# Kernel optimization log

Hardware: AMD Instinct MI355X
Metric: run time of the kernel (lower is better)

## Reference

```python
import jax, jax.numpy as jnp
import numpy as np

N_NODES = 40000
N_EDGES = 300000
EMBED = 256
LN_EPS = 1e-5
LEAKY_SLOPE = 0.01


def setup_inputs() -> dict:
    key = jax.random.key(0)
    ks = jax.random.split(key, 5)
    H = jax.random.normal(ks[0], (N_NODES, EMBED), dtype=jnp.float32)
    E = jax.random.normal(ks[1], (N_EDGES, EMBED), dtype=jnp.float32)
    ht = jax.random.randint(ks[2], (N_EDGES, 2), 0, N_NODES, dtype=jnp.int64)
    # Linear weights in torch convention: [out_features, in_features]
    W_fwd = jax.random.normal(ks[3], (EMBED, 2 * EMBED), dtype=jnp.float32) * (1.0 / np.sqrt(2 * EMBED))
    W_back = jax.random.normal(ks[4], (EMBED, 2 * EMBED), dtype=jnp.float32) * (1.0 / np.sqrt(2 * EMBED))
    return {
        "H": H,
        "E": E,
        "ht": ht,
        "queries": jnp.zeros((1,), jnp.float32),            # unused (message_weighting_function=None)
        "influence_weights": jnp.zeros((1,), jnp.float32),  # modeled as None
        "W_fwd": W_fwd,
        "b_fwd": jnp.zeros((EMBED,), jnp.float32),
        "W_back": W_back,
        "b_back": jnp.zeros((EMBED,), jnp.float32),
        "ln_w": jnp.ones((EMBED,), jnp.float32),
        "ln_b": jnp.zeros((EMBED,), jnp.float32),
    }


def _layer_norm(x, w, b):
    mu = jnp.mean(x, axis=-1, keepdims=True)
    var = jnp.mean(jnp.square(x - mu), axis=-1, keepdims=True)  # biased, as torch LayerNorm
    return (x - mu) * jax.lax.rsqrt(var + LN_EPS) * w + b


def reference(H, E, ht, queries, influence_weights, W_fwd, b_fwd, W_back, b_back, ln_w, ln_b):
    # queries / influence_weights are None in the modeled configuration; ignored.
    heads = ht[:, 0]
    tails = ht[:, 1]
    n = H.shape[0]
    # gather -> concat -> linear (messages in both edge directions)
    msg_fwd = jnp.concatenate([H[heads], E], axis=1) @ W_fwd.T + b_fwd    # [m, d]
    msg_back = jnp.concatenate([H[tails], E], axis=1) @ W_back.T + b_back  # [m, d]
    # scatter-add aggregate: fwd messages go to tails, back messages to heads
    msg_dst = jnp.concatenate([tails, heads], axis=0)          # [2m]
    messages = jnp.concatenate([msg_fwd, msg_back], axis=0)    # [2m, d]
    agg = jax.ops.segment_sum(messages, msg_dst, num_segments=n)  # [n, d]
    counts = jax.ops.segment_sum(jnp.ones_like(msg_dst, dtype=H.dtype), msg_dst, num_segments=n)
    agg = agg / counts[:, None]
    out = _layer_norm(jax.nn.leaky_relu(agg, LEAKY_SLOPE) + H, ln_w, ln_b)
    return out
```

## Files before the change

kernel.cpp:

```cpp
#include <hip/hip_runtime.h>
#include <hip/hip_bf16.h>

#define N_NODES 40000
#define N_EDGES 300000
#define EMBED 256
#define CAP 64

typedef __attribute__((ext_vector_type(8))) short s16x8;
typedef __attribute__((ext_vector_type(4))) float f32x4;

__device__ __forceinline__ float b2f(unsigned short u) {
    union { unsigned int i; float f; } v; v.i = ((unsigned int)u) << 16; return v.f;
}
__device__ __forceinline__ unsigned short f2b(float f) {
    unsigned int x = __float_as_uint(f);
    x += 0x7fffu + ((x >> 16) & 1u);
    return (unsigned short)(x >> 16);
}
__device__ __forceinline__ bool ht_is_i64(const int* __restrict__ ht) {
    int o = 0;
    #pragma unroll
    for (int k = 1; k < 16; k += 2) o |= ht[k];
    return o == 0;
}
__device__ __forceinline__ int clampN(int v) {
    unsigned u = (unsigned)v;
    return (u < N_NODES) ? v : 0;
}

__global__ __launch_bounds__(256) void convert_kernel(
    const float* __restrict__ H, const float* __restrict__ Wf,
    const float* __restrict__ Wb,
    unsigned short* __restrict__ Hbf, unsigned short* __restrict__ Wcat)
{
    constexpr int NH4 = (N_NODES * EMBED) / 4;
    constexpr int NW4 = (EMBED * 2 * EMBED) / 4;
    int ci = blockIdx.x * 256 + threadIdx.x;
    const float* src; unsigned short* dst;
    if (ci < NH4) {
        src = &H[(size_t)ci * 4]; dst = &Hbf[(size_t)ci * 4];
    } else if (ci < NH4 + NW4) {
        int j = (ci - NH4) * 4; int n = j >> 9, k = j & 511;
        src = &Wf[j]; dst = &Wcat[(size_t)n * 1024 + k];
    } else if (ci < NH4 + 2 * NW4) {
        int j = (ci - NH4 - NW4) * 4; int n = j >> 9, k = j & 511;
        src = &Wb[j]; dst = &Wcat[(size_t)n * 1024 + 512 + k];
    } else return;
    float4 v = *(const float4*)src;
    ushort4 o; o.x = f2b(v.x); o.y = f2b(v.y); o.z = f2b(v.z); o.w = f2b(v.w);
    *(ushort4*)dst = o;
}

__global__ __launch_bounds__(256) void build_kernel(
    const int* __restrict__ ht,
    int* __restrict__ cntf, int* __restrict__ cntb,
    int* __restrict__ listf, int* __restrict__ listb)
{
    int e = blockIdx.x * 256 + threadIdx.x;
    if (e >= N_EDGES) return;
    const bool wide = ht_is_i64(ht);
    int head = clampN(wide ? ht[(size_t)4 * e]     : ht[2 * e]);
    int tail = clampN(wide ? ht[(size_t)4 * e + 2] : ht[2 * e + 1]);
    int pf = atomicAdd(&cntf[tail], 1);
    if (pf < CAP) listf[tail * CAP + pf] = e;
    int pb = atomicAdd(&cntb[head], 1);
    if (pb < CAP) listb[head * CAP + pb] = e;
}

__global__ __launch_bounds__(256) void fused_kernel(
    const unsigned short* __restrict__ Hbf, const float* __restrict__ E,
    const int* __restrict__ ht, const unsigned short* __restrict__ Wcat,
    const float* __restrict__ bf_, const float* __restrict__ bb_,
    const float* __restrict__ H, const float* __restrict__ lw,
    const float* __restrict__ lb,
    const int* __restrict__ cntf, const int* __restrict__ cntb,
    const int* __restrict__ listf, const int* __restrict__ listb,
    float* __restrict__ out)
{
    constexpr int LDK = 1032;
    __shared__ unsigned short S[16 * LDK];
    __shared__ float stats[16][4][2];

    const int tid  = threadIdx.x;
    const int wid  = tid >> 6;
    const int lane = tid & 63;
    const int q    = lane >> 4;
    const int c    = lane & 15;
    const int m0   = blockIdx.x * 16;
    const bool wide = ht_is_i64(ht);

    for (int i = 0; i < 4; i++) {
        const int r    = wid * 4 + i;
        const int node = m0 + r;
        float aHf[4] = {0.f,0.f,0.f,0.f}, aEf[4] = {0.f,0.f,0.f,0.f};
        float aHb[4] = {0.f,0.f,0.f,0.f}, aEb[4] = {0.f,0.f,0.f,0.f};

        const int nf = min(cntf[node], CAP);
        for (int t = 0; t < nf; t++) {
            int e = listf[node * CAP + t];
            float4 e4 = *(const float4*)(&E[(size_t)e * EMBED + lane * 4]);
            int head = clampN(wide ? ht[(size_t)4 * e] : ht[2 * e]);
            ushort4 h4 = *(const ushort4*)(&Hbf[(size_t)head * EMBED + lane * 4]);
            aHf[0] += b2f(h4.x); aHf[1] += b2f(h4.y); aHf[2] += b2f(h4.z); aHf[3] += b2f(h4.w);
            aEf[0] += e4.x; aEf[1] += e4.y; aEf[2] += e4.z; aEf[3] += e4.w;
        }
        const int nb = min(cntb[node], CAP);
        for (int t = 0; t < nb; t++) {
            int e = listb[node * CAP + t];
            float4 e4 = *(const float4*)(&E[(size_t)e * EMBED + lane * 4]);
            int tail = clampN(wide ? ht[(size_t)4 * e + 2] : ht[2 * e + 1]);
            ushort4 h4 = *(const ushort4*)(&Hbf[(size_t)tail * EMBED + lane * 4]);
            aHb[0] += b2f(h4.x); aHb[1] += b2f(h4.y); aHb[2] += b2f(h4.z); aHb[3] += b2f(h4.w);
            aEb[0] += e4.x; aEb[1] += e4.y; aEb[2] += e4.z; aEb[3] += e4.w;
        }
        ushort4 o;
        o.x=f2b(aHf[0]); o.y=f2b(aHf[1]); o.z=f2b(aHf[2]); o.w=f2b(aHf[3]);
        *(ushort4*)(&S[r * LDK +   0 + lane * 4]) = o;
        o.x=f2b(aEf[0]); o.y=f2b(aEf[1]); o.z=f2b(aEf[2]); o.w=f2b(aEf[3]);
        *(ushort4*)(&S[r * LDK + 256 + lane * 4]) = o;
        o.x=f2b(aHb[0]); o.y=f2b(aHb[1]); o.z=f2b(aHb[2]); o.w=f2b(aHb[3]);
        *(ushort4*)(&S[r * LDK + 512 + lane * 4]) = o;
        o.x=f2b(aEb[0]); o.y=f2b(aEb[1]); o.z=f2b(aEb[2]); o.w=f2b(aEb[3]);
        *(ushort4*)(&S[r * LDK + 768 + lane * 4]) = o;
    }
    __syncthreads();

    const int n0 = wid * 64;
    f32x4 acc[4];
    #pragma unroll
    for (int nt = 0; nt < 4; nt++) acc[nt] = (f32x4){0.f,0.f,0.f,0.f};

    #pragma unroll 4
    for (int k0 = 0; k0 < 1024; k0 += 32) {
        s16x8 a = *(const s16x8*)(&S[c * LDK + k0 + q * 8]);
        #pragma unroll
        for (int nt = 0; nt < 4; nt++) {
            s16x8 b = *(const s16x8*)(&Wcat[(size_t)(n0 + nt * 16 + c) * 1024 + k0 + q * 8]);
            acc[nt] = __builtin_amdgcn_mfma_f32_16x16x32_bf16(a, b, acc[nt], 0, 0, 0);
        }
    }

    float x[4][4];
    float sr[4], ssr[4];
    #pragma unroll
    for (int reg = 0; reg < 4; reg++) {
        const int row  = q * 4 + reg;
        const int node = m0 + row;
        const float cf = (float)cntf[node];
        const float cb = (float)cntb[node];
        const float tot = cf + cb;
        const float inv = (tot > 0.f) ? (1.0f / tot) : 0.f;
        float s = 0.f, ss = 0.f;
        #pragma unroll
        for (int nt = 0; nt < 4; nt++) {
            const int j = n0 + nt * 16 + c;
            float v = acc[nt][reg] + cf * bf_[j] + cb * bb_[j];
            float m = v * inv;
            m = (m > 0.f) ? m : 0.01f * m;
            float xx = m + H[(size_t)node * EMBED + j];
            x[reg][nt] = xx; s += xx; ss += xx * xx;
        }
        sr[reg] = s; ssr[reg] = ss;
    }
    #pragma unroll
    for (int off = 1; off < 16; off <<= 1) {
        #pragma unroll
        for (int reg = 0; reg < 4; reg++) {
            sr[reg]  += __shfl_xor(sr[reg],  off);
            ssr[reg] += __shfl_xor(ssr[reg], off);
        }
    }
    if (c == 0) {
        #pragma unroll
        for (int reg = 0; reg < 4; reg++) {
            stats[q * 4 + reg][wid][0] = sr[reg];
            stats[q * 4 + reg][wid][1] = ssr[reg];
        }
    }
    __syncthreads();
    #pragma unroll
    for (int reg = 0; reg < 4; reg++) {
        const int row  = q * 4 + reg;
        const int node = m0 + row;
        float s  = stats[row][0][0] + stats[row][1][0] + stats[row][2][0] + stats[row][3][0];
        float ss = stats[row][0][1] + stats[row][1][1] + stats[row][2][1] + stats[row][3][1];
        const float mean = s * (1.0f / EMBED);
        float var = ss * (1.0f / EMBED) - mean * mean;
        var = var < 0.f ? 0.f : var;
        const float rstd = rsqrtf(var + 1e-5f);
        #pragma unroll
        for (int nt = 0; nt < 4; nt++) {
            const int j = n0 + nt * 16 + c;
            out[(size_t)node * EMBED + j] = (x[reg][nt] - mean) * rstd * lw[j] + lb[j];
        }
    }
}

extern "C" void kernel_launch(void* const* d_in, const int* in_sizes, int n_in,
                              void* d_out, int out_size, void* d_ws, size_t ws_size,
                              hipStream_t stream) {
    const float* H   = (const float*)d_in[0];
    const float* E   = (const float*)d_in[1];
    const int*   ht  = (const int*)d_in[2];
    const float* Wf  = (const float*)d_in[5];
    const float* bf_ = (const float*)d_in[6];
    const float* Wb  = (const float*)d_in[7];
    const float* bb_ = (const float*)d_in[8];
    const float* lw  = (const float*)d_in[9];
    const float* lb  = (const float*)d_in[10];
    float* out = (float*)d_out;

    int* cntf  = (int*)d_ws;
    int* cntb  = cntf + 40960;
    int* listf = cntb + 40960;
    int* listb = listf + N_NODES * CAP;
    unsigned short* Hbf  = (unsigned short*)(listb + N_NODES * CAP);
    unsigned short* Wcat = Hbf + (size_t)N_NODES * EMBED;

    hipMemsetAsync(d_ws, 0, 2 * 40960 * sizeof(int), stream);

    constexpr int NCHUNK = (N_NODES * EMBED + 2 * EMBED * 2 * EMBED) / 4;
    convert_kernel<<<(NCHUNK + 255) / 256, 256, 0, stream>>>(H, Wf, Wb, Hbf, Wcat);
    build_kernel<<<(N_EDGES + 255) / 256, 256, 0, stream>>>(ht, cntf, cntb, listf, listb);
    fused_kernel<<<N_NODES / 16, 256, 0, stream>>>(Hbf, E, ht, Wcat, bf_, bb_,
                                                   H, lw, lb, cntf, cntb,
                                                   listf, listb, out);
}
```

Baseline: 854.1 us.

## Prefetch edge lists into lanes and batch gathers eight-wide with readlane

Each wave now loads all edge-list entries and neighbor indices for its four nodes into registers up front, one lane per edge, then broadcasts them with readlane. The gather loop issues eight independent E and H row loads before accumulating, using zero weights to mask the tail of each batch. This replaces the serialized dependent index loads per edge with more memory-level parallelism, and the launch bounds add a minimum occupancy hint. The cost is extra register pressure and some wasted loads of padded edges, which read edge 0 and its head or tail node.

```diff
diff --git a/kernel.cpp b/kernel.cpp
--- a/kernel.cpp
+++ b/kernel.cpp
@@ -67,7 +67,7 @@
     if (pb < CAP) listb[head * CAP + pb] = e;
 }
 
-__global__ __launch_bounds__(256) void fused_kernel(
+__global__ __launch_bounds__(256, 4) void fused_kernel(
     const unsigned short* __restrict__ Hbf, const float* __restrict__ E,
     const int* __restrict__ ht, const unsigned short* __restrict__ Wcat,
     const float* __restrict__ bf_, const float* __restrict__ bb_,
@@ -89,39 +89,80 @@
     const int m0   = blockIdx.x * 16;
     const bool wide = ht_is_i64(ht);
 
-    for (int i = 0; i < 4; i++) {
-        const int r    = wid * 4 + i;
-        const int node = m0 + r;
+    int cF[4], cB[4];
+    int eF[4], eB[4], nF[4], nB[4];
+    #pragma unroll
+    for (int i = 0; i < 4; i++) {
+        const int node = m0 + wid * 4 + i;
+        cF[i] = min(cntf[node], CAP);
+        cB[i] = min(cntb[node], CAP);
+    }
+    #pragma unroll
+    for (int i = 0; i < 4; i++) {
+        const int node = m0 + wid * 4 + i;
+        eF[i] = (lane < cF[i]) ? listf[node * CAP + lane] : 0;
+        eB[i] = (lane < cB[i]) ? listb[node * CAP + lane] : 0;
+    }
+    #pragma unroll
+    for (int i = 0; i < 4; i++) {
+        nF[i] = clampN(wide ? ht[(size_t)4 * eF[i]]     : ht[2 * eF[i]]);
+        nB[i] = clampN(wide ? ht[(size_t)4 * eB[i] + 2] : ht[2 * eB[i] + 1]);
+    }
+
+    const int loff = lane * 4;
+
+    #pragma unroll
+    for (int i = 0; i < 4; i++) {
+        const int r = wid * 4 + i;
         float aHf[4] = {0.f,0.f,0.f,0.f}, aEf[4] = {0.f,0.f,0.f,0.f};
         float aHb[4] = {0.f,0.f,0.f,0.f}, aEb[4] = {0.f,0.f,0.f,0.f};
 
-        const int nf = min(cntf[node], CAP);
-        for (int t = 0; t < nf; t++) {
-            int e = listf[node * CAP + t];
-            float4 e4 = *(const float4*)(&E[(size_t)e * EMBED + lane * 4]);
-            int head = clampN(wide ? ht[(size_t)4 * e] : ht[2 * e]);
-            ushort4 h4 = *(const ushort4*)(&Hbf[(size_t)head * EMBED + lane * 4]);
-            aHf[0] += b2f(h4.x); aHf[1] += b2f(h4.y); aHf[2] += b2f(h4.z); aHf[3] += b2f(h4.w);
-            aEf[0] += e4.x; aEf[1] += e4.y; aEf[2] += e4.z; aEf[3] += e4.w;
-        }
-        const int nb = min(cntb[node], CAP);
-        for (int t = 0; t < nb; t++) {
-            int e = listb[node * CAP + t];
-            float4 e4 = *(const float4*)(&E[(size_t)e * EMBED + lane * 4]);
-            int tail = clampN(wide ? ht[(size_t)4 * e + 2] : ht[2 * e + 1]);
-            ushort4 h4 = *(const ushort4*)(&Hbf[(size_t)tail * EMBED + lane * 4]);
-            aHb[0] += b2f(h4.x); aHb[1] += b2f(h4.y); aHb[2] += b2f(h4.z); aHb[3] += b2f(h4.w);
-            aEb[0] += e4.x; aEb[1] += e4.y; aEb[2] += e4.z; aEb[3] += e4.w;
-        }
+        for (int t = 0; t < cF[i]; t += 8) {
+            float4 ev[8]; ushort4 hv[8]; float w[8];
+            #pragma unroll
+            for (int u = 0; u < 8; u++) {
+                const int e  = __builtin_amdgcn_readlane(eF[i], t + u);
+                const int nb = __builtin_amdgcn_readlane(nF[i], t + u);
+                w[u] = (t + u < cF[i]) ? 1.0f : 0.0f;
+                ev[u] = *(const float4*)(&E[(size_t)e * EMBED + loff]);
+                hv[u] = *(const ushort4*)(&Hbf[(size_t)nb * EMBED + loff]);
+            }
+            #pragma unroll
+            for (int u = 0; u < 8; u++) {
+                aEf[0] += w[u] * ev[u].x; aEf[1] += w[u] * ev[u].y;
+                aEf[2] += w[u] * ev[u].z; aEf[3] += w[u] * ev[u].w;
+                aHf[0] += w[u] * b2f(hv[u].x); aHf[1] += w[u] * b2f(hv[u].y);
+                aHf[2] += w[u] * b2f(hv[u].z); aHf[3] += w[u] * b2f(hv[u].w);
+            }
+        }
+        for (int t = 0; t < cB[i]; t += 8) {
+            float4 ev[8]; ushort4 hv[8]; float w[8];
+            #pragma unroll
+            for (int u = 0; u < 8; u++) {
+                const int e  = __builtin_amdgcn_readlane(eB[i], t + u);
+                const int nb = __builtin_amdgcn_readlane(nB[i], t + u);
+                w[u] = (t + u < cB[i]) ? 1.0f : 0.0f;
+                ev[u] = *(const float4*)(&E[(size_t)e * EMBED + loff]);
+                hv[u] = *(const ushort4*)(&Hbf[(size_t)nb * EMBED + loff]);
+            }
+            #pragma unroll
+            for (int u = 0; u < 8; u++) {
+                aEb[0] += w[u] * ev[u].x; aEb[1] += w[u] * ev[u].y;
+                aEb[2] += w[u] * ev[u].z; aEb[3] += w[u] * ev[u].w;
+                aHb[0] += w[u] * b2f(hv[u].x); aHb[1] += w[u] * b2f(hv[u].y);
+                aHb[2] += w[u] * b2f(hv[u].z); aHb[3] += w[u] * b2f(hv[u].w);
+            }
+        }
+
         ushort4 o;
         o.x=f2b(aHf[0]); o.y=f2b(aHf[1]); o.z=f2b(aHf[2]); o.w=f2b(aHf[3]);
-        *(ushort4*)(&S[r * LDK +   0 + lane * 4]) = o;
+        *(ushort4*)(&S[r * LDK +   0 + loff]) = o;
         o.x=f2b(aEf[0]); o.y=f2b(aEf[1]); o.z=f2b(aEf[2]); o.w=f2b(aEf[3]);
-        *(ushort4*)(&S[r * LDK + 256 + lane * 4]) = o;
+        *(ushort4*)(&S[r * LDK + 256 + loff]) = o;
         o.x=f2b(aHb[0]); o.y=f2b(aHb[1]); o.z=f2b(aHb[2]); o.w=f2b(aHb[3]);
-        *(ushort4*)(&S[r * LDK + 512 + lane * 4]) = o;
+        *(ushort4*)(&S[r * LDK + 512 + loff]) = o;
         o.x=f2b(aEb[0]); o.y=f2b(aEb[1]); o.z=f2b(aEb[2]); o.w=f2b(aEb[3]);
-        *(ushort4*)(&S[r * LDK + 768 + lane * 4]) = o;
+        *(ushort4*)(&S[r * LDK + 768 + loff]) = o;
     }
     __syncthreads();
 
```

After: 687.4 us. 1.24x faster.
